# Kernel tuning notes

Hardware: AMD Instinct MI355X
Metric: run time of the kernel (lower is better)

Reference implementation:

```python
import jax, jax.numpy as jnp
import numpy as np

B = 2
NUM_CLS = 20
NUM_DIM = 256
H = W = 448
FH = FW = 28
K_TOP = 25


def _l2norm(x, eps=1e-12):
    # matches torch F.normalize(dim=1): x / max(||x||, eps); zero rows stay zero
    return x / jnp.maximum(jnp.linalg.norm(x, axis=-1, keepdims=True), eps)


def setup_inputs():
    key = jax.random.key(0)
    k1, k2, k3, k4 = jax.random.split(key, 4)
    fmap = jax.random.normal(k1, (B, NUM_DIM, FH, FW), jnp.float32)
    cam = jax.random.uniform(k2, (B, NUM_CLS, H, W), jnp.float32)
    cls_label = jax.random.randint(k3, (B, NUM_CLS), 0, 2).astype(jnp.float32)
    proj_weight = jax.random.normal(k4, (NUM_CLS, NUM_DIM), jnp.float32) * 0.02
    feature_contrast = jnp.zeros((NUM_CLS, NUM_DIM), jnp.float32)
    return {"fmap": fmap, "cam": cam, "cls_label": cls_label,
            "proj_weight": proj_weight, "feature_contrast": feature_contrast,
            "hig_thre": 0.7, "low_thre": 0.25, "bg_thre": 0.5}


def _forward(fmap, cam, cls_label, proj_weight, feature_contrast, hig_thre, low_thre, bg_thre):
    b, c, h, w = cam.shape
    d = fmap.shape[1]
    dt = fmap.dtype

    # ---- pseudo-label generation (vectorized over b,h,w) ----
    valid_cam = cls_label[:, :, None, None] * cam                       # [B,C,H,W]
    top2_v, top2_i = jax.lax.top_k(jnp.moveaxis(valid_cam, 1, -1), 2)   # [B,H,W,2]
    top1, second = top2_v[..., 0], top2_v[..., 1]
    pseudo = top2_i[..., 0] + 1
    pseudo = jnp.where(top1 < hig_thre, 255, pseudo)
    pseudo = jnp.where(top1 < low_thre, 0, pseudo)
    pseudo = jnp.where(top1 < bg_thre, 0, pseudo)
    pseudo = jnp.where((top1 - second < 0.3) & (top1 > hig_thre), 255, pseudo)

    # ---- upsample features (bilinear, align_corners=False) ----
    fmap_up = jax.image.resize(fmap, (b, d, h, w), 'bilinear')
    fmap_flat = fmap_up.reshape(b, d, h * w)                            # [B,D,HW]
    pseudo_flat = pseudo.reshape(b, h * w)                              # [B,HW]

    # ---- per-class features, both branches computed densely then selected ----
    cls_ids = jnp.arange(c) + 1
    mask = (pseudo_flat[:, None, :] == cls_ids[None, :, None]).astype(dt)  # [B,C,HW]
    counts = mask.sum(-1)                                                  # [B,C]
    feat_mask = jnp.einsum('bcp,bdp->bcd', mask, fmap_flat) / jnp.maximum(counts, 1.0)[:, :, None]
    _, top_idx = jax.lax.top_k(valid_cam.reshape(b, c, h * w), K_TOP)      # [B,C,25]
    gathered = jnp.take_along_axis(fmap_flat[:, None, :, :], top_idx[:, :, None, :], axis=-1)  # [B,C,D,25]
    feat_topk = gathered.mean(-1)                                          # [B,C,D]
    present = cls_label > 0.5                                              # [B,C] bool
    fsm = jnp.where((counts == 0.0)[:, :, None], feat_topk, feat_mask) * present[:, :, None]

    eye_f = jnp.eye(c, dtype=dt)
    eye_b = jnp.eye(c, dtype=bool)

    # ---- sequential per-sample loop (EMA memory bank carried across batch) ----
    def step(carry, xs):
        fc, loss_cls, loss_ccf = carry
        fsm_i, present_i = xs                                    # [C,D], [C]
        fsm_n = _l2norm(fsm_i)
        fc_n = _l2norm(jax.lax.stop_gradient(fc))
        cos = jnp.clip(jnp.abs(fsm_n @ fc_n.T), 1e-5, 1.0 - 1e-5)  # [C,C]
        ident = jnp.diag(present_i.astype(dt))
        loss_ccf = loss_ccf - (ident * jnp.log(cos) + (1.0 - ident) * jnp.log1p(-cos)).mean()
        off_max = jnp.where(eye_b, -jnp.inf, cos).max(axis=1)      # max over j != c
        qualify = present_i & (off_max < 0.6)                      # [C] bool
        p = jax.nn.softmax(fsm_i @ proj_weight.T, axis=-1)         # [C,C]
        logp = jnp.maximum(jnp.log(p), -100.0)
        log1mp = jnp.maximum(jnp.log1p(-p), -100.0)
        term = -(eye_f * logp + (1.0 - eye_f) * log1mp).mean(axis=-1)  # BCE(softmax, onehot) per class
        loss_cls = loss_cls + jnp.sum(jnp.where(qualify, term, 0.0))
        n = qualify.sum().astype(dt)
        loss_cls = jnp.where(n > 0, loss_cls / jnp.maximum(n, 1.0), loss_cls)
        fc = jnp.where(qualify[:, None], 0.95 * fc + 0.05 * jax.lax.stop_gradient(fsm_i), fc)
        return (fc, loss_cls, loss_ccf), None

    zero = jnp.asarray(0.0, dt)
    (_, loss_cls, loss_ccf), _ = jax.lax.scan(step, (feature_contrast, zero, zero), (fsm, present))
    return loss_ccf + loss_cls


def reference(fmap, cam, cls_label, proj_weight, feature_contrast, hig_thre, low_thre, bg_thre):
    return _forward(fmap, cam, cls_label, proj_weight, feature_contrast, hig_thre, low_thre, bg_thre)
```

## Files before the change

### kernel.cpp

```cpp
#include <hip/hip_runtime.h>
#include <cstdint>

#define HW 200704
#define IMG_W 448
#define NCLS 20
#define NDIM 256
#define NB2 784
#define LK 260

#define ASYNC_COPY4(gp, lp)                                                    \
  __builtin_amdgcn_global_load_lds(                                            \
      (const __attribute__((address_space(1))) void*)(gp),                     \
      (__attribute__((address_space(3))) void*)(lp), 4, 0, 0)

__global__ __launch_bounds__(256) void k_front(const float* __restrict__ fmap,
                                               float* __restrict__ fmapT,
                                               const float* __restrict__ cam,
                                               const float* __restrict__ cls_label,
                                               const float* __restrict__ hig_p,
                                               const float* __restrict__ low_p,
                                               const float* __restrict__ bg_p,
                                               float* __restrict__ W) {
  __shared__ float sT[NCLS][256];
  int tid = threadIdx.x;

  if (blockIdx.x >= 2 * NB2) {
    float (*tile)[33] = (float (*)[33]) & sT[0][0];
    int blk = blockIdx.x - 2 * NB2;
    int b = blk / 200;
    int t = blk % 200;
    int dT = t / 25, sT2 = t % 25;
    int ty = tid >> 5, tx = tid & 31;
#pragma unroll
    for (int r = 0; r < 4; ++r) {
      int d = dT * 32 + ty + r * 8;
      int s = sT2 * 32 + tx;
      if (s < 784) tile[ty + r * 8][tx] = fmap[((size_t)(b * 256 + d)) * 784 + s];
    }
    __syncthreads();
#pragma unroll
    for (int r = 0; r < 4; ++r) {
      int s = sT2 * 32 + ty + r * 8;
      int d = dT * 32 + tx;
      if (s < 784) fmapT[((size_t)(b * 784 + s)) * 256 + d] = tile[tx][ty + r * 8];
    }
    return;
  }

  int b = blockIdx.x / NB2;
  int blkInB = blockIdx.x % NB2;
  int pix0 = blkInB * 256;
  int wave = tid >> 6, lane = tid & 63;

  bool pres = (lane < NCLS) && (cls_label[b * NCLS + lane] != 0.0f);
  unsigned long long pm = __ballot(pres);
  unsigned mask = (unsigned)(pm & 0xFFFFFu);
  int np = __popc(mask);
  const float* camb = cam + (size_t)b * NCLS * HW + pix0 + wave * 64 + lane;

  {
    unsigned m = mask;
    for (int k = 0; k < np; ++k) {
      int c = __builtin_ctz(m); m &= m - 1u;
      ASYNC_COPY4(camb + (size_t)c * HW, &sT[k][wave * 64]);
    }
  }
  __builtin_amdgcn_s_waitcnt(0);

  float top1 = -1.0f, sec = -1.0f;
  int cls1 = 0;
  {
    unsigned m = mask;
    for (int k = 0; k < np; ++k) {
      int c = __builtin_ctz(m); m &= m - 1u;
      float x = sT[k][tid];
      bool gt = x > top1;
      sec = gt ? top1 : fmaxf(sec, fminf(x, top1));
      cls1 = gt ? c : cls1;
      top1 = gt ? x : top1;
    }
  }
  if (np < NCLS) sec = fmaxf(sec, 0.0f);
  float hig = hig_p[0], low = low_p[0], bg = bg_p[0];
  int pix = pix0 + tid;
  int ps = cls1 + 1;
  if (top1 < hig) ps = 255;
  if (top1 < low) ps = 0;
  if (top1 < bg)  ps = 0;
  if ((top1 - sec < 0.3f) && (top1 > hig)) ps = 255;
  if (ps >= 1 && ps <= NCLS) {
    int cls = ps - 1;
    int y = pix / IMG_W, x = pix % IMG_W;
    float sy = (y + 0.5f) * 0.0625f - 0.5f; sy = fminf(fmaxf(sy, 0.0f), 27.0f);
    float sx = (x + 0.5f) * 0.0625f - 0.5f; sx = fminf(fmaxf(sx, 0.0f), 27.0f);
    int fy0 = (int)sy, fx0 = (int)sx;
    int fy1 = min(fy0 + 1, 27), fx1 = min(fx0 + 1, 27);
    float wy = sy - (float)fy0, wx = sx - (float)fx0;
    float* Wb = W + (size_t)(b * NCLS + cls) * 784;
    atomicAdd(&Wb[fy0 * 28 + fx0], (1.0f - wy) * (1.0f - wx));
    atomicAdd(&Wb[fy0 * 28 + fx1], (1.0f - wy) * wx);
    atomicAdd(&Wb[fy1 * 28 + fx0], wy * (1.0f - wx));
    atomicAdd(&Wb[fy1 * 28 + fx1], wy * wx);
  }
}

__global__ __launch_bounds__(512) void k_feat(const float* __restrict__ fmapT,
                                              const float* __restrict__ cam,
                                              const float* __restrict__ Wg,
                                              const float* __restrict__ cls_label,
                                              float* __restrict__ P,
                                              float* __restrict__ S,
                                              float* __restrict__ cntW) {
  __shared__ float sW[784];
  __shared__ float sH[2][256];
  __shared__ float sRed[8];
  __shared__ float sCntf;
  __shared__ float wv[8]; __shared__ int wi[8];
  __shared__ float selV; __shared__ int selI;
  __shared__ int sTop[25];
  int bc = blockIdx.x >> 2, part = blockIdx.x & 3;
  int b = bc / NCLS;
  int tid = threadIdx.x;
  int dim = tid & 255, h = tid >> 8;
  if (cls_label[bc] == 0.0f) return;

  for (int s = tid; s < 784; s += 512) sW[s] = Wg[(size_t)bc * 784 + s];
  __syncthreads();
  {
    float cs = sW[tid >= 512 ? 0 : tid];
    cs = (tid < 512) ? sW[tid] : 0.0f;
    if (tid < 272) cs += sW[tid + 512];
    for (int off = 32; off > 0; off >>= 1) cs += __shfl_xor(cs, off, 64);
    if ((tid & 63) == 0) sRed[tid >> 6] = cs;
    __syncthreads();
    if (tid == 0) {
      float s = 0.0f;
      for (int w = 0; w < 8; ++w) s += sRed[w];
      sCntf = s;
    }
    __syncthreads();
  }
  float cntf = sCntf;
  const float* fT = fmapT + (size_t)b * 784 * 256;

  if (cntf > 0.0f) {
    int s0 = part * 196;
    if (h == 0) {
      float a0 = 0.0f, a1 = 0.0f;
      for (int s = s0; s < s0 + 196; s += 4) {
        a0 += sW[s]     * fT[(size_t)(s)     * 256 + dim];
        a1 += sW[s + 1] * fT[(size_t)(s + 1) * 256 + dim];
      }
      sH[0][dim] = a0 + a1;
    } else {
      float a2 = 0.0f, a3 = 0.0f;
      for (int s = s0; s < s0 + 196; s += 4) {
        a2 += sW[s + 2] * fT[(size_t)(s + 2) * 256 + dim];
        a3 += sW[s + 3] * fT[(size_t)(s + 3) * 256 + dim];
      }
      sH[1][dim] = a2 + a3;
    }
    __syncthreads();
    if (tid < 256)
      P[(size_t)(bc * 4 + part) * 256 + tid] = sH[0][tid] + sH[1][tid];
    if (part == 0 && tid == 0) cntW[bc] = cntf;
  } else if (part == 0) {
    if (tid == 0) cntW[bc] = 0.0f;
    const float* camc = cam + (size_t)bc * HW;
    float lastV = 3.0e38f; int lastI = -1;
    for (int r = 0; r < 25; ++r) {
      float bv = -1.0e30f; int bi = 0x7fffffff;
      for (int p = tid; p < HW; p += 512) {
        float vv2 = camc[p];
        if (((vv2 < lastV) || (vv2 == lastV && p > lastI)) &&
            ((vv2 > bv) || (vv2 == bv && p < bi))) { bv = vv2; bi = p; }
      }
      for (int off = 32; off > 0; off >>= 1) {
        float ov = __shfl_xor(bv, off, 64);
        int   oi = __shfl_xor(bi, off, 64);
        if (ov > bv || (ov == bv && oi < bi)) { bv = ov; bi = oi; }
      }
      if ((tid & 63) == 0) { wv[tid >> 6] = bv; wi[tid >> 6] = bi; }
      __syncthreads();
      if (tid == 0) {
        for (int w = 1; w < 8; ++w)
          if (wv[w] > bv || (wv[w] == bv && wi[w] < bi)) { bv = wv[w]; bi = wi[w]; }
        selV = bv; selI = bi; sTop[r] = bi;
      }
      __syncthreads();
      lastV = selV; lastI = selI;
    }
    if (tid < 256) {
      float at = 0.0f;
      for (int r = 0; r < 25; ++r) {
        int p = sTop[r];
        int y = p / IMG_W, x = p % IMG_W;
        float sy = (y + 0.5f) * 0.0625f - 0.5f; sy = fminf(fmaxf(sy, 0.0f), 27.0f);
        float sx = (x + 0.5f) * 0.0625f - 0.5f; sx = fminf(fmaxf(sx, 0.0f), 27.0f);
        int fy0 = (int)sy, fx0 = (int)sx;
        int fy1 = min(fy0 + 1, 27), fx1 = min(fx0 + 1, 27);
        float wy = sy - (float)fy0, wx = sx - (float)fx0;
        at += (1.0f - wy) * (1.0f - wx) * fT[(size_t)(fy0 * 28 + fx0) * 256 + tid]
            + (1.0f - wy) * wx          * fT[(size_t)(fy0 * 28 + fx1) * 256 + tid]
            + wy          * (1.0f - wx) * fT[(size_t)(fy1 * 28 + fx0) * 256 + tid]
            + wy          * wx          * fT[(size_t)(fy1 * 28 + fx1) * 256 + tid];
      }
      S[(size_t)bc * 256 + tid] = at * (1.0f / 25.0f);
    }
  }
}

__global__ __launch_bounds__(1024) void k_loss(const float* __restrict__ P,
                                               const float* __restrict__ S,
                                               const float* __restrict__ cntW,
                                               const float* __restrict__ cls_label,
                                               const float* __restrict__ proj_w,
                                               const float* __restrict__ fc_init,
                                               float* __restrict__ out) {
  __shared__ float sFsm[2][NCLS * LK];
  __shared__ float sFc[NCLS * LK], sPw[NCLS * LK];
  __shared__ float sLogit[2][400], sCos[400];
  __shared__ float sBCE[2][NCLS], sRow[NCLS];
  __shared__ float sNormI[2][NCLS], sNormC[NCLS];
  __shared__ int   sZI[2][NCLS], sZC[NCLS], sQual[NCLS];
  __shared__ float sPres[2][NCLS];
  __shared__ float sScal[2];
  int tid = threadIdx.x;

  for (int idx = tid; idx < 2 * NCLS * NDIM; idx += 1024) {
    int bc = idx >> 8, d = idx & 255;
    float v = 0.0f;
    if (cls_label[bc] != 0.0f) {
      float c = cntW[bc];
      if (c > 0.0f) {
        const float* p = P + (size_t)bc * 1024 + d;
        v = ((p[0] + p[256]) + (p[512] + p[768])) / fmaxf(c, 1.0f);
      } else {
        v = S[(size_t)bc * 256 + d];
      }
    }
    sFsm[bc / NCLS][(bc % NCLS) * LK + d] = v;
  }
  for (int idx = tid; idx < NCLS * NDIM; idx += 1024) {
    int r = idx >> 8, d = idx & 255;
    sFc[r * LK + d] = fc_init[idx];
    sPw[r * LK + d] = proj_w[idx];
  }
  if (tid < 40) sPres[tid / NCLS][tid % NCLS] = cls_label[tid];
  if (tid == 0) { sScal[0] = 0.0f; sScal[1] = 0.0f; }
  __syncthreads();

  if (tid < 800) {
    int b = tid / 400, pi = tid % 400;
    int i = pi / NCLS, j = pi % NCLS;
    const float* ra = &sFsm[b][i * LK];
    const float* rb = &sPw[j * LK];
    float a0 = 0, a1 = 0, a2 = 0, a3 = 0, a4 = 0, a5 = 0, a6 = 0, a7 = 0;
    for (int d = 0; d < 256; d += 16) {
      float4 x0 = *(const float4*)&ra[d],      y0 = *(const float4*)&rb[d];
      float4 x1 = *(const float4*)&ra[d + 4],  y1 = *(const float4*)&rb[d + 4];
      float4 x2 = *(const float4*)&ra[d + 8],  y2 = *(const float4*)&rb[d + 8];
      float4 x3 = *(const float4*)&ra[d + 12], y3 = *(const float4*)&rb[d + 12];
      a0 += x0.x * y0.x + x0.y * y0.y;  a1 += x0.z * y0.z + x0.w * y0.w;
      a2 += x1.x * y1.x + x1.y * y1.y;  a3 += x1.z * y1.z + x1.w * y1.w;
      a4 += x2.x * y2.x + x2.y * y2.y;  a5 += x2.z * y2.z + x2.w * y2.w;
      a6 += x3.x * y3.x + x3.y * y3.y;  a7 += x3.z * y3.z + x3.w * y3.w;
    }
    sLogit[b][pi] = ((a0 + a1) + (a2 + a3)) + ((a4 + a5) + (a6 + a7));
  }
  __syncthreads();

  {
    int g = tid >> 3, sub = tid & 7;
    if (g < 60) {
      const float* row = (g < 40) ? &sFsm[g / NCLS][(g % NCLS) * LK] : &sFc[(g - 40) * LK];
      float a0 = 0.0f, a1 = 0.0f, a2 = 0.0f, a3 = 0.0f;
      int d0 = sub * 32;
#pragma unroll
      for (int d = d0; d < d0 + 32; d += 8) {
        float4 x = *(const float4*)&row[d];
        float4 y = *(const float4*)&row[d + 4];
        a0 += x.x * x.x + x.y * x.y;
        a1 += x.z * x.z + x.w * x.w;
        a2 += y.x * y.x + y.y * y.y;
        a3 += y.z * y.z + y.w * y.w;
      }
      float s = (a0 + a1) + (a2 + a3);
      s += __shfl_xor(s, 1, 64);
      s += __shfl_xor(s, 2, 64);
      s += __shfl_xor(s, 4, 64);
      if (sub == 0) {
        if (g < 40) { sNormI[g / NCLS][g % NCLS] = fmaxf(sqrtf(s), 1e-12f); sZI[g / NCLS][g % NCLS] = (s == 0.0f); }
        else { sNormC[g - 40] = fmaxf(sqrtf(s), 1e-12f); sZC[g - 40] = (s == 0.0f); }
      }
    }
  }
  __syncthreads();

  {
    int team = tid >> 5, jj = tid & 31;
    for (int r = team; r < 40; r += 32) {
      int b = r / NCLS, i = r % NCLS;
      float l = (jj < NCLS) ? sLogit[b][i * NCLS + jj] : -3.0e38f;
      float m = l;
#pragma unroll
      for (int off = 1; off < 32; off <<= 1) m = fmaxf(m, __shfl_xor(m, off, 64));
      float e = (jj < NCLS) ? expf(l - m) : 0.0f;
      float sS = e;
#pragma unroll
      for (int off = 1; off < 32; off <<= 1) sS += __shfl_xor(sS, off, 64);
      float term = 0.0f;
      if (jj < NCLS) {
        float p = e / sS;
        term = (jj == i) ? fmaxf(logf(p), -100.0f) : fmaxf(log1pf(-p), -100.0f);
      }
#pragma unroll
      for (int off = 1; off < 32; off <<= 1) term += __shfl_xor(term, off, 64);
      if (jj == 0) sBCE[b][i] = -term / 20.0f;
    }
  }
  __syncthreads();

  for (int b = 0; b < 2; ++b) {
    if (b == 1) {
      int g = tid >> 3, sub = tid & 7;
      if (g < NCLS) {
        const float* row = &sFc[g * LK];
        float a0 = 0.0f, a1 = 0.0f, a2 = 0.0f, a3 = 0.0f;
        int d0 = sub * 32;
#pragma unroll
        for (int d = d0; d < d0 + 32; d += 8) {
          float4 x = *(const float4*)&row[d];
          float4 y = *(const float4*)&row[d + 4];
          a0 += x.x * x.x + x.y * x.y;
          a1 += x.z * x.z + x.w * x.w;
          a2 += y.x * y.x + y.y * y.y;
          a3 += y.z * y.z + y.w * y.w;
        }
        float s = (a0 + a1) + (a2 + a3);
        s += __shfl_xor(s, 1, 64);
        s += __shfl_xor(s, 2, 64);
        s += __shfl_xor(s, 4, 64);
        if (sub == 0) { sNormC[g] = fmaxf(sqrtf(s), 1e-12f); sZC[g] = (s == 0.0f); }
      }
      __syncthreads();
    }
    {
      int pair = tid >> 1, sub = tid & 1;
      if (pair < 400) {
        int i = pair / NCLS, j = pair % NCLS;
        float c0;
        if (sZI[b][i] || sZC[j]) c0 = 0.0f;
        else {
          const float* ra = &sFsm[b][i * LK];
          const float* rb = &sFc[j * LK];
          float a0 = 0.0f, a1 = 0.0f, a2 = 0.0f, a3 = 0.0f;
          int d0 = sub * 128;
          for (int d = d0; d < d0 + 128; d += 8) {
            float4 x  = *(const float4*)&ra[d];
            float4 y  = *(const float4*)&rb[d];
            float4 x2 = *(const float4*)&ra[d + 4];
            float4 y2 = *(const float4*)&rb[d + 4];
            a0 += x.x * y.x + x.y * y.y;
            a1 += x.z * y.z + x.w * y.w;
            a2 += x2.x * y2.x + x2.y * y2.y;
            a3 += x2.z * y2.z + x2.w * y2.w;
          }
          float acc = (a0 + a1) + (a2 + a3);
          acc += __shfl_xor(acc, 1, 64);
          c0 = fabsf(acc / (sNormI[b][i] * sNormC[j]));
        }
        if (sub == 0) sCos[pair] = fminf(fmaxf(c0, 1e-5f), 1.0f - 1e-5f);
      }
    }
    __syncthreads();
    {
      int i = tid >> 5, jj = tid & 31;
      if (i < NCLS) {
        float pres = (sPres[b][i] > 0.5f) ? 1.0f : 0.0f;
        float contrib = 0.0f, omv = -3.0e38f;
        if (jj < NCLS) {
          float c0 = sCos[i * NCLS + jj];
          float ident = (jj == i) ? pres : 0.0f;
          contrib = ident * logf(c0) + (1.0f - ident) * log1pf(-c0);
          if (jj != i) omv = c0;
        }
#pragma unroll
        for (int off = 1; off < 32; off <<= 1) {
          contrib += __shfl_xor(contrib, off, 64);
          omv = fmaxf(omv, __shfl_xor(omv, off, 64));
        }
        if (jj == 0) { sRow[i] = contrib; sQual[i] = (pres > 0.5f && omv < 0.6f) ? 1 : 0; }
      }
    }
    __syncthreads();
    if (tid == 0) {
      float s = 0.0f;
      for (int r = 0; r < NCLS; ++r) s += sRow[r];
      sScal[0] -= s / 400.0f;
      float add = 0.0f; int nq = 0;
      for (int r = 0; r < NCLS; ++r) if (sQual[r]) { add += sBCE[b][r]; nq++; }
      float lc = sScal[1] + add;
      if (nq > 0) lc = lc / fmaxf((float)nq, 1.0f);
      sScal[1] = lc;
    }
    for (int idx = tid; idx < NCLS * NDIM; idx += 1024) {
      int r = idx >> 8, d = idx & 255;
      if (sQual[r]) sFc[r * LK + d] = 0.95f * sFc[r * LK + d] + 0.05f * sFsm[b][r * LK + d];
    }
    __syncthreads();
  }
  if (tid == 0) out[0] = sScal[0] + sScal[1];
}

extern "C" void kernel_launch(void* const* d_in, const int* in_sizes, int n_in,
                              void* d_out, int out_size, void* d_ws, size_t ws_size,
                              hipStream_t stream) {
  const float* fmap      = (const float*)d_in[0];
  const float* cam       = (const float*)d_in[1];
  const float* cls_label = (const float*)d_in[2];
  const float* proj_w    = (const float*)d_in[3];
  const float* fc_init   = (const float*)d_in[4];
  const float* hig       = (const float*)d_in[5];
  const float* low       = (const float*)d_in[6];
  const float* bg        = (const float*)d_in[7];
  float* out = (float*)d_out;

  char* ws = (char*)d_ws;
  float* W     = (float*)(ws);
  float* cntW  = (float*)(ws + 125440);
  float* P     = (float*)(ws + 125600);
  float* S     = (float*)(ws + 289440);
  float* fmapT = (float*)(ws + 330400);

  hipMemsetAsync(ws, 0, 125440, stream);
  k_front<<<2 * NB2 + 400,  256, 0, stream>>>(fmap, fmapT, cam, cls_label,
                                              hig, low, bg, W);
  k_feat <<<          160,  512, 0, stream>>>(fmapT, cam, W, cls_label, P, S, cntW);
  k_loss <<<            1, 1024, 0, stream>>>(P, S, cntW, cls_label, proj_w, fc_init, out);
}
```

Before: 123.7 us.

## Fuse feature and loss kernels with last-block-done atomic counter

Merges the per-class feature reduction kernel and the single-block loss kernel into one launch. Each block bumps a global counter after finishing its feature work, and the last block to arrive runs the loss computation. Block size goes from 512 to 1024 threads, so the weighted sum splits four ways and the top-k scan uses a wider stride. The aim is to remove one kernel launch and its gap. The cost is large shared memory per block, which limits occupancy, plus a serial tail that waits on the slowest block.

```diff
diff --git a/kernel.cpp b/kernel.cpp
--- a/kernel.cpp
+++ b/kernel.cpp
@@ -104,119 +104,25 @@
   }
 }
 
-__global__ __launch_bounds__(512) void k_feat(const float* __restrict__ fmapT,
-                                              const float* __restrict__ cam,
-                                              const float* __restrict__ Wg,
-                                              const float* __restrict__ cls_label,
-                                              float* __restrict__ P,
-                                              float* __restrict__ S,
-                                              float* __restrict__ cntW) {
+__global__ __launch_bounds__(1024) void k_feat_loss(const float* __restrict__ fmapT,
+                                                    const float* __restrict__ cam,
+                                                    const float* __restrict__ Wg,
+                                                    const float* __restrict__ cls_label,
+                                                    const float* __restrict__ proj_w,
+                                                    const float* __restrict__ fc_init,
+                                                    int* __restrict__ done,
+                                                    float* __restrict__ P,
+                                                    float* __restrict__ S,
+                                                    float* __restrict__ cntW,
+                                                    float* __restrict__ out) {
   __shared__ float sW[784];
-  __shared__ float sH[2][256];
-  __shared__ float sRed[8];
+  __shared__ float sH[4][256];
+  __shared__ float sRed[16];
   __shared__ float sCntf;
-  __shared__ float wv[8]; __shared__ int wi[8];
+  __shared__ float wv[16]; __shared__ int wi[16];
   __shared__ float selV; __shared__ int selI;
   __shared__ int sTop[25];
-  int bc = blockIdx.x >> 2, part = blockIdx.x & 3;
-  int b = bc / NCLS;
-  int tid = threadIdx.x;
-  int dim = tid & 255, h = tid >> 8;
-  if (cls_label[bc] == 0.0f) return;
-
-  for (int s = tid; s < 784; s += 512) sW[s] = Wg[(size_t)bc * 784 + s];
-  __syncthreads();
-  {
-    float cs = sW[tid >= 512 ? 0 : tid];
-    cs = (tid < 512) ? sW[tid] : 0.0f;
-    if (tid < 272) cs += sW[tid + 512];
-    for (int off = 32; off > 0; off >>= 1) cs += __shfl_xor(cs, off, 64);
-    if ((tid & 63) == 0) sRed[tid >> 6] = cs;
-    __syncthreads();
-    if (tid == 0) {
-      float s = 0.0f;
-      for (int w = 0; w < 8; ++w) s += sRed[w];
-      sCntf = s;
-    }
-    __syncthreads();
-  }
-  float cntf = sCntf;
-  const float* fT = fmapT + (size_t)b * 784 * 256;
-
-  if (cntf > 0.0f) {
-    int s0 = part * 196;
-    if (h == 0) {
-      float a0 = 0.0f, a1 = 0.0f;
-      for (int s = s0; s < s0 + 196; s += 4) {
-        a0 += sW[s]     * fT[(size_t)(s)     * 256 + dim];
-        a1 += sW[s + 1] * fT[(size_t)(s + 1) * 256 + dim];
-      }
-      sH[0][dim] = a0 + a1;
-    } else {
-      float a2 = 0.0f, a3 = 0.0f;
-      for (int s = s0; s < s0 + 196; s += 4) {
-        a2 += sW[s + 2] * fT[(size_t)(s + 2) * 256 + dim];
-        a3 += sW[s + 3] * fT[(size_t)(s + 3) * 256 + dim];
-      }
-      sH[1][dim] = a2 + a3;
-    }
-    __syncthreads();
-    if (tid < 256)
-      P[(size_t)(bc * 4 + part) * 256 + tid] = sH[0][tid] + sH[1][tid];
-    if (part == 0 && tid == 0) cntW[bc] = cntf;
-  } else if (part == 0) {
-    if (tid == 0) cntW[bc] = 0.0f;
-    const float* camc = cam + (size_t)bc * HW;
-    float lastV = 3.0e38f; int lastI = -1;
-    for (int r = 0; r < 25; ++r) {
-      float bv = -1.0e30f; int bi = 0x7fffffff;
-      for (int p = tid; p < HW; p += 512) {
-        float vv2 = camc[p];
-        if (((vv2 < lastV) || (vv2 == lastV && p > lastI)) &&
-            ((vv2 > bv) || (vv2 == bv && p < bi))) { bv = vv2; bi = p; }
-      }
-      for (int off = 32; off > 0; off >>= 1) {
-        float ov = __shfl_xor(bv, off, 64);
-        int   oi = __shfl_xor(bi, off, 64);
-        if (ov > bv || (ov == bv && oi < bi)) { bv = ov; bi = oi; }
-      }
-      if ((tid & 63) == 0) { wv[tid >> 6] = bv; wi[tid >> 6] = bi; }
-      __syncthreads();
-      if (tid == 0) {
-        for (int w = 1; w < 8; ++w)
-          if (wv[w] > bv || (wv[w] == bv && wi[w] < bi)) { bv = wv[w]; bi = wi[w]; }
-        selV = bv; selI = bi; sTop[r] = bi;
-      }
-      __syncthreads();
-      lastV = selV; lastI = selI;
-    }
-    if (tid < 256) {
-      float at = 0.0f;
-      for (int r = 0; r < 25; ++r) {
-        int p = sTop[r];
-        int y = p / IMG_W, x = p % IMG_W;
-        float sy = (y + 0.5f) * 0.0625f - 0.5f; sy = fminf(fmaxf(sy, 0.0f), 27.0f);
-        float sx = (x + 0.5f) * 0.0625f - 0.5f; sx = fminf(fmaxf(sx, 0.0f), 27.0f);
-        int fy0 = (int)sy, fx0 = (int)sx;
-        int fy1 = min(fy0 + 1, 27), fx1 = min(fx0 + 1, 27);
-        float wy = sy - (float)fy0, wx = sx - (float)fx0;
-        at += (1.0f - wy) * (1.0f - wx) * fT[(size_t)(fy0 * 28 + fx0) * 256 + tid]
-            + (1.0f - wy) * wx          * fT[(size_t)(fy0 * 28 + fx1) * 256 + tid]
-            + wy          * (1.0f - wx) * fT[(size_t)(fy1 * 28 + fx0) * 256 + tid]
-            + wy          * wx          * fT[(size_t)(fy1 * 28 + fx1) * 256 + tid];
-      }
-      S[(size_t)bc * 256 + tid] = at * (1.0f / 25.0f);
-    }
-  }
-}
-
-__global__ __launch_bounds__(1024) void k_loss(const float* __restrict__ P,
-                                               const float* __restrict__ S,
-                                               const float* __restrict__ cntW,
-                                               const float* __restrict__ cls_label,
-                                               const float* __restrict__ proj_w,
-                                               const float* __restrict__ fc_init,
-                                               float* __restrict__ out) {
+  __shared__ int sLast;
   __shared__ float sFsm[2][NCLS * LK];
   __shared__ float sFc[NCLS * LK], sPw[NCLS * LK];
   __shared__ float sLogit[2][400], sCos[400];
@@ -225,21 +131,109 @@
   __shared__ int   sZI[2][NCLS], sZC[NCLS], sQual[NCLS];
   __shared__ float sPres[2][NCLS];
   __shared__ float sScal[2];
+
+  int bc = blockIdx.x >> 2, part = blockIdx.x & 3;
+  int b = bc / NCLS;
   int tid = threadIdx.x;
+  int dim = tid & 255, h = tid >> 8;
+
+  if (cls_label[bc] != 0.0f) {
+    for (int s = tid; s < 784; s += 1024) sW[s] = Wg[(size_t)bc * 784 + s];
+    __syncthreads();
+    {
+      float cs = (tid < 784) ? sW[tid] : 0.0f;
+      for (int off = 32; off > 0; off >>= 1) cs += __shfl_xor(cs, off, 64);
+      if ((tid & 63) == 0) sRed[tid >> 6] = cs;
+      __syncthreads();
+      if (tid == 0) {
+        float s = 0.0f;
+        for (int w = 0; w < 16; ++w) s += sRed[w];
+        sCntf = s;
+      }
+      __syncthreads();
+    }
+    float cntf = sCntf;
+    const float* fT = fmapT + (size_t)b * 784 * 256;
+
+    if (cntf > 0.0f) {
+      int s0 = part * 196;
+      float a = 0.0f;
+      for (int s = s0 + h; s < s0 + 196; s += 4)
+        a += sW[s] * fT[(size_t)s * 256 + dim];
+      sH[h][dim] = a;
+      __syncthreads();
+      if (tid < 256)
+        P[(size_t)(bc * 4 + part) * 256 + tid] =
+            (sH[0][tid] + sH[1][tid]) + (sH[2][tid] + sH[3][tid]);
+      if (part == 0 && tid == 0) cntW[bc] = cntf;
+    } else if (part == 0) {
+      if (tid == 0) cntW[bc] = 0.0f;
+      const float* camc = cam + (size_t)bc * HW;
+      float lastV = 3.0e38f; int lastI = -1;
+      for (int r = 0; r < 25; ++r) {
+        float bv = -1.0e30f; int bi = 0x7fffffff;
+        for (int p = tid; p < HW; p += 1024) {
+          float vv2 = camc[p];
+          if (((vv2 < lastV) || (vv2 == lastV && p > lastI)) &&
+              ((vv2 > bv) || (vv2 == bv && p < bi))) { bv = vv2; bi = p; }
+        }
+        for (int off = 32; off > 0; off >>= 1) {
+          float ov = __shfl_xor(bv, off, 64);
+          int   oi = __shfl_xor(bi, off, 64);
+          if (ov > bv || (ov == bv && oi < bi)) { bv = ov; bi = oi; }
+        }
+        if ((tid & 63) == 0) { wv[tid >> 6] = bv; wi[tid >> 6] = bi; }
+        __syncthreads();
+        if (tid == 0) {
+          for (int w = 1; w < 16; ++w)
+            if (wv[w] > bv || (wv[w] == bv && wi[w] < bi)) { bv = wv[w]; bi = wi[w]; }
+          selV = bv; selI = bi; sTop[r] = bi;
+        }
+        __syncthreads();
+        lastV = selV; lastI = selI;
+      }
+      if (tid < 256) {
+        float at = 0.0f;
+        for (int r = 0; r < 25; ++r) {
+          int p = sTop[r];
+          int y = p / IMG_W, x = p % IMG_W;
+          float sy = (y + 0.5f) * 0.0625f - 0.5f; sy = fminf(fmaxf(sy, 0.0f), 27.0f);
+          float sx = (x + 0.5f) * 0.0625f - 0.5f; sx = fminf(fmaxf(sx, 0.0f), 27.0f);
+          int fy0 = (int)sy, fx0 = (int)sx;
+          int fy1 = min(fy0 + 1, 27), fx1 = min(fx0 + 1, 27);
+          float wy = sy - (float)fy0, wx = sx - (float)fx0;
+          at += (1.0f - wy) * (1.0f - wx) * fT[(size_t)(fy0 * 28 + fx0) * 256 + tid]
+              + (1.0f - wy) * wx          * fT[(size_t)(fy0 * 28 + fx1) * 256 + tid]
+              + wy          * (1.0f - wx) * fT[(size_t)(fy1 * 28 + fx0) * 256 + tid]
+              + wy          * wx          * fT[(size_t)(fy1 * 28 + fx1) * 256 + tid];
+        }
+        S[(size_t)bc * 256 + tid] = at * (1.0f / 25.0f);
+      }
+    }
+  }
+  __syncthreads();
+  if (tid == 0) {
+    __threadfence();
+    int t = atomicAdd(done, 1);
+    sLast = (t == 159) ? 1 : 0;
+  }
+  __syncthreads();
+  if (!sLast) return;
+  __threadfence();
 
   for (int idx = tid; idx < 2 * NCLS * NDIM; idx += 1024) {
-    int bc = idx >> 8, d = idx & 255;
+    int bcc = idx >> 8, d = idx & 255;
     float v = 0.0f;
-    if (cls_label[bc] != 0.0f) {
-      float c = cntW[bc];
+    if (cls_label[bcc] != 0.0f) {
+      float c = cntW[bcc];
       if (c > 0.0f) {
-        const float* p = P + (size_t)bc * 1024 + d;
+        const float* p = P + (size_t)bcc * 1024 + d;
         v = ((p[0] + p[256]) + (p[512] + p[768])) / fmaxf(c, 1.0f);
       } else {
-        v = S[(size_t)bc * 256 + d];
-      }
-    }
-    sFsm[bc / NCLS][(bc % NCLS) * LK + d] = v;
+        v = S[(size_t)bcc * 256 + d];
+      }
+    }
+    sFsm[bcc / NCLS][(bcc % NCLS) * LK + d] = v;
   }
   for (int idx = tid; idx < NCLS * NDIM; idx += 1024) {
     int r = idx >> 8, d = idx & 255;
@@ -251,9 +245,9 @@
   __syncthreads();
 
   if (tid < 800) {
-    int b = tid / 400, pi = tid % 400;
+    int bb = tid / 400, pi = tid % 400;
     int i = pi / NCLS, j = pi % NCLS;
-    const float* ra = &sFsm[b][i * LK];
+    const float* ra = &sFsm[bb][i * LK];
     const float* rb = &sPw[j * LK];
     float a0 = 0, a1 = 0, a2 = 0, a3 = 0, a4 = 0, a5 = 0, a6 = 0, a7 = 0;
     for (int d = 0; d < 256; d += 16) {
@@ -266,7 +260,7 @@
       a4 += x2.x * y2.x + x2.y * y2.y;  a5 += x2.z * y2.z + x2.w * y2.w;
       a6 += x3.x * y3.x + x3.y * y3.y;  a7 += x3.z * y3.z + x3.w * y3.w;
     }
-    sLogit[b][pi] = ((a0 + a1) + (a2 + a3)) + ((a4 + a5) + (a6 + a7));
+    sLogit[bb][pi] = ((a0 + a1) + (a2 + a3)) + ((a4 + a5) + (a6 + a7));
   }
   __syncthreads();
 
@@ -300,8 +294,8 @@
   {
     int team = tid >> 5, jj = tid & 31;
     for (int r = team; r < 40; r += 32) {
-      int b = r / NCLS, i = r % NCLS;
-      float l = (jj < NCLS) ? sLogit[b][i * NCLS + jj] : -3.0e38f;
+      int bb = r / NCLS, i = r % NCLS;
+      float l = (jj < NCLS) ? sLogit[bb][i * NCLS + jj] : -3.0e38f;
       float m = l;
 #pragma unroll
       for (int off = 1; off < 32; off <<= 1) m = fmaxf(m, __shfl_xor(m, off, 64));
@@ -316,13 +310,13 @@
       }
 #pragma unroll
       for (int off = 1; off < 32; off <<= 1) term += __shfl_xor(term, off, 64);
-      if (jj == 0) sBCE[b][i] = -term / 20.0f;
-    }
-  }
-  __syncthreads();
-
-  for (int b = 0; b < 2; ++b) {
-    if (b == 1) {
+      if (jj == 0) sBCE[bb][i] = -term / 20.0f;
+    }
+  }
+  __syncthreads();
+
+  for (int bb = 0; bb < 2; ++bb) {
+    if (bb == 1) {
       int g = tid >> 3, sub = tid & 7;
       if (g < NCLS) {
         const float* row = &sFc[g * LK];
@@ -350,9 +344,9 @@
       if (pair < 400) {
         int i = pair / NCLS, j = pair % NCLS;
         float c0;
-        if (sZI[b][i] || sZC[j]) c0 = 0.0f;
+        if (sZI[bb][i] || sZC[j]) c0 = 0.0f;
         else {
-          const float* ra = &sFsm[b][i * LK];
+          const float* ra = &sFsm[bb][i * LK];
           const float* rb = &sFc[j * LK];
           float a0 = 0.0f, a1 = 0.0f, a2 = 0.0f, a3 = 0.0f;
           int d0 = sub * 128;
@@ -368,7 +362,7 @@
           }
           float acc = (a0 + a1) + (a2 + a3);
           acc += __shfl_xor(acc, 1, 64);
-          c0 = fabsf(acc / (sNormI[b][i] * sNormC[j]));
+          c0 = fabsf(acc / (sNormI[bb][i] * sNormC[j]));
         }
         if (sub == 0) sCos[pair] = fminf(fmaxf(c0, 1e-5f), 1.0f - 1e-5f);
       }
@@ -377,7 +371,7 @@
     {
       int i = tid >> 5, jj = tid & 31;
       if (i < NCLS) {
-        float pres = (sPres[b][i] > 0.5f) ? 1.0f : 0.0f;
+        float pres = (sPres[bb][i] > 0.5f) ? 1.0f : 0.0f;
         float contrib = 0.0f, omv = -3.0e38f;
         if (jj < NCLS) {
           float c0 = sCos[i * NCLS + jj];
@@ -399,14 +393,14 @@
       for (int r = 0; r < NCLS; ++r) s += sRow[r];
       sScal[0] -= s / 400.0f;
       float add = 0.0f; int nq = 0;
-      for (int r = 0; r < NCLS; ++r) if (sQual[r]) { add += sBCE[b][r]; nq++; }
+      for (int r = 0; r < NCLS; ++r) if (sQual[r]) { add += sBCE[bb][r]; nq++; }
       float lc = sScal[1] + add;
       if (nq > 0) lc = lc / fmaxf((float)nq, 1.0f);
       sScal[1] = lc;
     }
     for (int idx = tid; idx < NCLS * NDIM; idx += 1024) {
       int r = idx >> 8, d = idx & 255;
-      if (sQual[r]) sFc[r * LK + d] = 0.95f * sFc[r * LK + d] + 0.05f * sFsm[b][r * LK + d];
+      if (sQual[r]) sFc[r * LK + d] = 0.95f * sFc[r * LK + d] + 0.05f * sFsm[bb][r * LK + d];
     }
     __syncthreads();
   }
@@ -428,14 +422,15 @@
 
   char* ws = (char*)d_ws;
   float* W     = (float*)(ws);
-  float* cntW  = (float*)(ws + 125440);
-  float* P     = (float*)(ws + 125600);
-  float* S     = (float*)(ws + 289440);
-  float* fmapT = (float*)(ws + 330400);
-
-  hipMemsetAsync(ws, 0, 125440, stream);
-  k_front<<<2 * NB2 + 400,  256, 0, stream>>>(fmap, fmapT, cam, cls_label,
-                                              hig, low, bg, W);
-  k_feat <<<          160,  512, 0, stream>>>(fmapT, cam, W, cls_label, P, S, cntW);
-  k_loss <<<            1, 1024, 0, stream>>>(P, S, cntW, cls_label, proj_w, fc_init, out);
+  int*   done  = (int*)  (ws + 125440);
+  float* cntW  = (float*)(ws + 125472);
+  float* P     = (float*)(ws + 125632);
+  float* S     = (float*)(ws + 289472);
+  float* fmapT = (float*)(ws + 330432);
+
+  hipMemsetAsync(ws, 0, 125472, stream);
+  k_front    <<<2 * NB2 + 400,  256, 0, stream>>>(fmap, fmapT, cam, cls_label,
+                                                  hig, low, bg, W);
+  k_feat_loss<<<          160, 1024, 0, stream>>>(fmapT, cam, W, cls_label,
+                                                  proj_w, fc_init, done, P, S, cntW, out);
 }
```

Result: slower. 140.1 us (+13.3%).
